# Kernel optimization log

Measured on AMD Instinct MI355X. Metric: run time of the kernel, lower is better.

Reference implementation:

```python
import jax, jax.numpy as jnp
import numpy as np

B, T, F = 256, 784, 1
H, D, C = 256, 1024, 10  # cell_size, dense_size, num_classes


def setup_inputs() -> dict:
    key = jax.random.key(0)
    ks = jax.random.split(key, 5)
    s = 0.05
    return {
        "X": jax.random.normal(ks[0], (B, T, F), jnp.float32),
        "W_lstm": jax.random.normal(ks[1], (F + H, 4 * H), jnp.float32) * s,
        "b_lstm": jnp.zeros((4 * H,), jnp.float32),
        "W_dense": jax.random.normal(ks[2], (H, D), jnp.float32) * s,
        "b_dense": jnp.zeros((D,), jnp.float32),
        "W_pred": jax.random.normal(ks[3], (D, C), jnp.float32) * s,
        "b_pred": jnp.zeros((C,), jnp.float32),
        "seq_length": T,
    }


def reference(X, W_lstm, b_lstm, W_dense, b_dense, W_pred, b_pred, seq_length):
    # TF LSTMCell: kernel [F+H, 4H], gate order (i, j, f, o), forget_bias=1.0
    b, t, f = X.shape
    h4 = W_lstm.shape[1]
    h = h4 // 4
    Wx, Wh = W_lstm[:f], W_lstm[f:]
    # Precompute input projections for all timesteps: [T, B, 4H]
    xproj = jnp.einsum('tbf,fg->tbg', jnp.transpose(X, (1, 0, 2)), Wx) + b_lstm

    def step(carry, xp):
        c, hst = carry
        gates = xp + hst @ Wh  # [B, 4H]
        i, j, fg, o = jnp.split(gates, 4, axis=-1)
        new_c = jax.nn.sigmoid(fg + 1.0) * c + jax.nn.sigmoid(i) * jnp.tanh(j)
        new_h = jax.nn.sigmoid(o) * jnp.tanh(new_c)
        return (new_c, new_h), None

    init = (jnp.zeros((b, h), X.dtype), jnp.zeros((b, h), X.dtype))
    (_, h_last), _ = jax.lax.scan(step, init, xproj)

    # Dropout in inference mode = identity
    dense = jax.nn.relu(h_last @ W_dense + b_dense)
    logits = dense @ W_pred + b_pred
    return logits
```

## Files before the change

kernel.cpp:

```cpp
#include <hip/hip_runtime.h>
#include <stdint.h>

#define TSEQ  784
#define BATCH 256
#define HID   256
#define DNS   1024
#define NCLS  10
#define NGRP  16
#define NSLC  8

typedef __attribute__((ext_vector_type(8))) short bf16x8_t;
typedef __attribute__((ext_vector_type(4))) float f32x4_t;

__device__ __forceinline__ float sigmoidf_(float x) { return 1.0f / (1.0f + __expf(-x)); }
__device__ __forceinline__ float tanhf_(float x) {
    float ax = fabsf(x);
    float e  = __expf(2.0f * ax);
    float r  = 1.0f - 2.0f / (e + 1.0f);
    return copysignf(r, x);
}
__device__ __forceinline__ uint32_t bf16rne(float f) {
    uint32_t u = __float_as_uint(f);
    return (u + 0x7FFFu + ((u >> 16) & 1u)) >> 16;
}
__device__ __forceinline__ float bf16tof(uint32_t h) { return __uint_as_float(h << 16); }

__global__ __launch_bounds__(256, 1)
void lstm_mfma(const float* __restrict__ X,
               const float* __restrict__ W_lstm,
               const float* __restrict__ b_lstm,
               uint32_t* __restrict__ hx,
               uint32_t* __restrict__ tags)
{
    __shared__ uint32_t WtU[32768];
    __shared__ uint32_t hA[4096];
    __shared__ float    gateL[4 * 32 * 17];

    const int tid  = threadIdx.x;
    const int lane = tid & 63;
    const int wid  = tid >> 6;
    const int cidx = lane & 15;
    const int kh   = lane >> 4;

    const int bid = blockIdx.x;
    const int s   = bid >> 4;
    const int g   = bid & 15;

    for (int idx = tid; idx < 8 * 16 * 128; idx += 256) {
        const int n  = idx >> 11;
        const int c  = (idx >> 7) & 15;
        const int dw = idx & 127;
        const int k0 = dw * 2;
        const int col = (n >> 1) * 256 + s * 32 + (n & 1) * 16 + c;
        const float w0 = W_lstm[(1 + k0) * 1024 + col];
        const float w1 = W_lstm[(2 + k0) * 1024 + col];
        const uint32_t h0 = bf16rne(w0), h1 = bf16rne(w1);
        const uint32_t l0 = bf16rne(w0 - bf16tof(h0));
        const uint32_t l1 = bf16rne(w1 - bf16tof(h1));
        const int kc = dw >> 2, rem = dw & 3;
        const int dwp = ((kc ^ (c & 7)) << 2) | rem;
        const int o = (n * 16 + c) * 128 + dwp;
        WtU[o]         = h0 | (h1 << 16);
        WtU[16384 + o] = l0 | (l1 << 16);
    }

    const int er = tid >> 4;
    const int eu = tid & 15;
    float wx0[4], wx1[4], bb0[4], bb1[4];
    #pragma unroll
    for (int q = 0; q < 4; ++q) {
        const int c0 = q * 256 + s * 32 + eu;
        wx0[q] = W_lstm[c0];      wx1[q] = W_lstm[c0 + 16];
        bb0[q] = b_lstm[c0];      bb1[q] = b_lstm[c0 + 16];
    }
    const float* xrow = X + (g * 16 + er) * TSEQ;
    float cc0 = 0.0f, cc1 = 0.0f;

    const int key = (cidx + (cidx >> 2)) & 3;
    const int kq  = (kh ^ key) << 2;

    __syncthreads();

    for (int t = 0; t < TSEQ; ++t) {
        if (t > 0 && wid == 0) {
            const uint32_t tt = (uint32_t)t;
            int guard = 1 << 22;
            bool ok;
            do {
                uint32_t v = __hip_atomic_load(&tags[g * 8 + (lane & 7)],
                                               __ATOMIC_RELAXED, __HIP_MEMORY_SCOPE_AGENT);
                ok = __all(v >= tt);
            } while (!ok && --guard);
        }
        __syncthreads();

        {
            const int bufr = t & 1;
            const unsigned long long* src =
                (const unsigned long long*)hx + (size_t)(bufr * NGRP + g) * 2048;
            unsigned long long v[8];
            #pragma unroll
            for (int j = 0; j < 8; ++j) {
                v[j] = __hip_atomic_load(&src[j * 256 + tid],
                                         __ATOMIC_RELAXED, __HIP_MEMORY_SCOPE_AGENT);
            }
            #pragma unroll
            for (int j = 0; j < 8; ++j) {
                const int m   = j * 256 + tid;
                const int kt  = m >> 8;
                const int lvl = (m >> 7) & 1;
                const int ci  = (m & 127) >> 3;
                const int ko  = (m & 7) * 2;
                const int khj = ko >> 2, dp = ko & 3;
                const int kyj = (ci + (ci >> 2)) & 3;
                const int dst = kt * 512 + lvl * 256 + ci * 16 + ((khj ^ kyj) << 2) + dp;
                *(unsigned long long*)&hA[dst] = v[j];
            }
        }
        __syncthreads();

        f32x4_t acc0 = {0.f, 0.f, 0.f, 0.f}, acc1 = acc0;
        #pragma unroll
        for (int kt = 0; kt < 8; ++kt) {
            bf16x8_t av_h = *reinterpret_cast<const bf16x8_t*>(&hA[kt * 512 + cidx * 16 + kq]);
            bf16x8_t av_l = *reinterpret_cast<const bf16x8_t*>(&hA[kt * 512 + 256 + cidx * 16 + kq]);
            const int kc = kt * 4 + kh;
            const int ob0 = ((wid * 2) * 16 + cidx) * 128 + ((kc ^ (cidx & 7)) << 2);
            const int ob1 = ((wid * 2 + 1) * 16 + cidx) * 128 + ((kc ^ (cidx & 7)) << 2);
            bf16x8_t bh0 = *reinterpret_cast<const bf16x8_t*>(&WtU[ob0]);
            bf16x8_t bl0 = *reinterpret_cast<const bf16x8_t*>(&WtU[16384 + ob0]);
            bf16x8_t bh1 = *reinterpret_cast<const bf16x8_t*>(&WtU[ob1]);
            bf16x8_t bl1 = *reinterpret_cast<const bf16x8_t*>(&WtU[16384 + ob1]);
            acc0 = __builtin_amdgcn_mfma_f32_16x16x32_bf16(av_h, bh0, acc0, 0, 0, 0);
            acc0 = __builtin_amdgcn_mfma_f32_16x16x32_bf16(av_h, bl0, acc0, 0, 0, 0);
            acc0 = __builtin_amdgcn_mfma_f32_16x16x32_bf16(av_l, bh0, acc0, 0, 0, 0);
            acc1 = __builtin_amdgcn_mfma_f32_16x16x32_bf16(av_h, bh1, acc1, 0, 0, 0);
            acc1 = __builtin_amdgcn_mfma_f32_16x16x32_bf16(av_h, bl1, acc1, 0, 0, 0);
            acc1 = __builtin_amdgcn_mfma_f32_16x16x32_bf16(av_l, bh1, acc1, 0, 0, 0);
        }

        #pragma unroll
        for (int reg = 0; reg < 4; ++reg) {
            gateL[(wid * 32 + cidx) * 17      + kh * 4 + reg] = acc0[reg];
            gateL[(wid * 32 + 16 + cidx) * 17 + kh * 4 + reg] = acc1[reg];
        }
        __syncthreads();

        const float xv = xrow[t];
        float g0[4], g1[4];
        #pragma unroll
        for (int q = 0; q < 4; ++q) {
            g0[q] = gateL[(q * 32 + eu) * 17 + er]      + xv * wx0[q] + bb0[q];
            g1[q] = gateL[(q * 32 + 16 + eu) * 17 + er] + xv * wx1[q] + bb1[q];
        }
        cc0 = fmaf(sigmoidf_(g0[2] + 1.0f), cc0, sigmoidf_(g0[0]) * tanhf_(g0[1]));
        const float h0 = sigmoidf_(g0[3]) * tanhf_(cc0);
        cc1 = fmaf(sigmoidf_(g1[2] + 1.0f), cc1, sigmoidf_(g1[0]) * tanhf_(g1[1]));
        const float h1 = sigmoidf_(g1[3]) * tanhf_(cc1);

        const float h0n = __shfl_xor(h0, 1, 64);
        const float h1n = __shfl_xor(h1, 1, 64);
        if ((eu & 1) == 0) {
            const int bufw  = (t + 1) & 1;
            const int basew = ((bufw * NGRP + g) * NSLC + s) * 512 + er * 16;
            const uint32_t hi0 = bf16rne(h0),  hi0n = bf16rne(h0n);
            const uint32_t hi1 = bf16rne(h1),  hi1n = bf16rne(h1n);
            const uint32_t lo0  = bf16rne(h0  - bf16tof(hi0));
            const uint32_t lo0n = bf16rne(h0n - bf16tof(hi0n));
            const uint32_t lo1  = bf16rne(h1  - bf16tof(hi1));
            const uint32_t lo1n = bf16rne(h1n - bf16tof(hi1n));
            const int D0 = eu >> 1, D1 = 8 + (eu >> 1);
            __hip_atomic_store(&hx[basew + D0], hi0 | (hi0n << 16),
                               __ATOMIC_RELAXED, __HIP_MEMORY_SCOPE_AGENT);
            __hip_atomic_store(&hx[basew + D1], hi1 | (hi1n << 16),
                               __ATOMIC_RELAXED, __HIP_MEMORY_SCOPE_AGENT);
            __hip_atomic_store(&hx[basew + 256 + D0], lo0 | (lo0n << 16),
                               __ATOMIC_RELAXED, __HIP_MEMORY_SCOPE_AGENT);
            __hip_atomic_store(&hx[basew + 256 + D1], lo1 | (lo1n << 16),
                               __ATOMIC_RELAXED, __HIP_MEMORY_SCOPE_AGENT);
        }
        __syncthreads();
        if (tid == 0) {
            __hip_atomic_store(&tags[g * 8 + s], (uint32_t)(t + 1),
                               __ATOMIC_RELAXED, __HIP_MEMORY_SCOPE_AGENT);
        }
    }
}

__global__ __launch_bounds__(256, 1)
void head_kernel(const uint32_t* __restrict__ hx,
                 const float* __restrict__ W_dense,
                 const float* __restrict__ b_dense,
                 const float* __restrict__ W_pred,
                 const float* __restrict__ b_pred,
                 float* __restrict__ out) {
    __shared__ float hs[HID];
    __shared__ float ds[DNS];
    __shared__ float red[4];

    const int b = blockIdx.x;
    const int g = b >> 4, er = b & 15;
    const int tid = threadIdx.x;

    {
        const int s  = tid >> 5;
        const int uu = tid & 31;
        const int base = (g * NSLC + s) * 512 + er * 16;
        const uint32_t dh = __hip_atomic_load(&hx[base + (uu >> 1)],
                                              __ATOMIC_RELAXED, __HIP_MEMORY_SCOPE_AGENT);
        const uint32_t dl = __hip_atomic_load(&hx[base + 256 + (uu >> 1)],
                                              __ATOMIC_RELAXED, __HIP_MEMORY_SCOPE_AGENT);
        const int sh = (uu & 1) * 16;
        hs[tid] = bf16tof((dh >> sh) & 0xFFFFu) + bf16tof((dl >> sh) & 0xFFFFu);
    }
    __syncthreads();

    for (int d = tid; d < DNS; d += 256) {
        float acc = b_dense[d];
        for (int k = 0; k < HID; k += 4) {
            float4 h4 = *reinterpret_cast<const float4*>(&hs[k]);
            acc = fmaf(h4.x, W_dense[(k + 0) * DNS + d], acc);
            acc = fmaf(h4.y, W_dense[(k + 1) * DNS + d], acc);
            acc = fmaf(h4.z, W_dense[(k + 2) * DNS + d], acc);
            acc = fmaf(h4.w, W_dense[(k + 3) * DNS + d], acc);
        }
        ds[d] = fmaxf(acc, 0.0f);
    }
    __syncthreads();

    const int wid = tid >> 6, lane = tid & 63;
    for (int c = 0; c < NCLS; ++c) {
        float p = 0.0f;
        for (int k = tid; k < DNS; k += 256) {
            p = fmaf(ds[k], W_pred[k * NCLS + c], p);
        }
        #pragma unroll
        for (int off = 32; off > 0; off >>= 1) {
            p += __shfl_down(p, off, 64);
        }
        if (lane == 0) red[wid] = p;
        __syncthreads();
        if (tid == 0) {
            out[b * NCLS + c] = red[0] + red[1] + red[2] + red[3] + b_pred[c];
        }
        __syncthreads();
    }
}

extern "C" void kernel_launch(void* const* d_in, const int* in_sizes, int n_in,
                              void* d_out, int out_size, void* d_ws, size_t ws_size,
                              hipStream_t stream) {
    const float* X       = (const float*)d_in[0];
    const float* W_lstm  = (const float*)d_in[1];
    const float* b_lstm  = (const float*)d_in[2];
    const float* W_dense = (const float*)d_in[3];
    const float* b_dense = (const float*)d_in[4];
    const float* W_pred  = (const float*)d_in[5];
    const float* b_pred  = (const float*)d_in[6];
    float* out = (float*)d_out;

    uint32_t* hx   = (uint32_t*)d_ws;
    uint32_t* tags = hx + 131072;

    hipMemsetAsync(hx, 0, NGRP * NSLC * 512 * sizeof(uint32_t), stream);
    hipMemsetAsync(tags, 0, NGRP * NSLC * sizeof(uint32_t), stream);

    lstm_mfma<<<NGRP * NSLC, 256, 0, stream>>>(X, W_lstm, b_lstm, hx, tags);
    head_kernel<<<BATCH, 256, 0, stream>>>(hx, W_dense, b_dense, W_pred, b_pred, out);
}
```

Baseline: 2.225 ms.

## Process two batch groups per block and load h operands directly from global

Halves the grid from 128 to 64 blocks, with each block handling two batch groups (A and B) over the same weight slice. Each weight fragment read from LDS now feeds twice the MFMA work, and each step waits on one tag poll. The recurrent h operand is now loaded straight from global into MFMA registers, removing the LDS staging pass and one barrier per step. The cost is more serial work per block on the critical recurrence path, fewer CUs in use, and higher register pressure.

New measurement: 4.983 ms. +124.0%, slower.

```diff
diff --git a/kernel.cpp b/kernel.cpp
--- a/kernel.cpp
+++ b/kernel.cpp
@@ -25,16 +25,21 @@
 }
 __device__ __forceinline__ float bf16tof(uint32_t h) { return __uint_as_float(h << 16); }
 
+union AF { uint32_t u[4]; unsigned long long q[2]; bf16x8_t v; };
+
+#define ALOAD(dst, ptr) \
+    dst = __hip_atomic_load((ptr), __ATOMIC_RELAXED, __HIP_MEMORY_SCOPE_AGENT)
+
 __global__ __launch_bounds__(256, 1)
-void lstm_mfma(const float* __restrict__ X,
-               const float* __restrict__ W_lstm,
-               const float* __restrict__ b_lstm,
-               uint32_t* __restrict__ hx,
-               uint32_t* __restrict__ tags)
+void lstm_mfma2(const float* __restrict__ X,
+                const float* __restrict__ W_lstm,
+                const float* __restrict__ b_lstm,
+                uint32_t* __restrict__ hx,
+                uint32_t* __restrict__ tags)
 {
     __shared__ uint32_t WtU[32768];
-    __shared__ uint32_t hA[4096];
-    __shared__ float    gateL[4 * 32 * 17];
+    __shared__ float    gateA[4 * 32 * 17];
+    __shared__ float    gateB[4 * 32 * 17];
 
     const int tid  = threadIdx.x;
     const int lane = tid & 63;
@@ -43,8 +48,9 @@
     const int kh   = lane >> 4;
 
     const int bid = blockIdx.x;
-    const int s   = bid >> 4;
-    const int g   = bid & 15;
+    const int s   = bid >> 3;
+    const int p   = bid & 7;
+    const int gA  = 2 * p, gB = 2 * p + 1;
 
     for (int idx = tid; idx < 8 * 16 * 128; idx += 256) {
         const int n  = idx >> 11;
@@ -73,11 +79,9 @@
         wx0[q] = W_lstm[c0];      wx1[q] = W_lstm[c0 + 16];
         bb0[q] = b_lstm[c0];      bb1[q] = b_lstm[c0 + 16];
     }
-    const float* xrow = X + (g * 16 + er) * TSEQ;
-    float cc0 = 0.0f, cc1 = 0.0f;
-
-    const int key = (cidx + (cidx >> 2)) & 3;
-    const int kq  = (kh ^ key) << 2;
+    const float* xrowA = X + (gA * 16 + er) * TSEQ;
+    const float* xrowB = X + (gB * 16 + er) * TSEQ;
+    float ccA0 = 0.f, ccA1 = 0.f, ccB0 = 0.f, ccB1 = 0.f;
 
     __syncthreads();
 
@@ -87,101 +91,133 @@
             int guard = 1 << 22;
             bool ok;
             do {
-                uint32_t v = __hip_atomic_load(&tags[g * 8 + (lane & 7)],
+                uint32_t v = __hip_atomic_load(&tags[p * 16 + (lane & 15)],
                                                __ATOMIC_RELAXED, __HIP_MEMORY_SCOPE_AGENT);
                 ok = __all(v >= tt);
             } while (!ok && --guard);
         }
         __syncthreads();
 
-        {
-            const int bufr = t & 1;
-            const unsigned long long* src =
-                (const unsigned long long*)hx + (size_t)(bufr * NGRP + g) * 2048;
-            unsigned long long v[8];
-            #pragma unroll
-            for (int j = 0; j < 8; ++j) {
-                v[j] = __hip_atomic_load(&src[j * 256 + tid],
-                                         __ATOMIC_RELAXED, __HIP_MEMORY_SCOPE_AGENT);
-            }
-            #pragma unroll
-            for (int j = 0; j < 8; ++j) {
-                const int m   = j * 256 + tid;
-                const int kt  = m >> 8;
-                const int lvl = (m >> 7) & 1;
-                const int ci  = (m & 127) >> 3;
-                const int ko  = (m & 7) * 2;
-                const int khj = ko >> 2, dp = ko & 3;
-                const int kyj = (ci + (ci >> 2)) & 3;
-                const int dst = kt * 512 + lvl * 256 + ci * 16 + ((khj ^ kyj) << 2) + dp;
-                *(unsigned long long*)&hA[dst] = v[j];
-            }
-        }
-        __syncthreads();
-
-        f32x4_t acc0 = {0.f, 0.f, 0.f, 0.f}, acc1 = acc0;
+        const int bufr = t & 1;
+        AF ahA[8], alA[8], ahB[8], alB[8];
         #pragma unroll
         for (int kt = 0; kt < 8; ++kt) {
-            bf16x8_t av_h = *reinterpret_cast<const bf16x8_t*>(&hA[kt * 512 + cidx * 16 + kq]);
-            bf16x8_t av_l = *reinterpret_cast<const bf16x8_t*>(&hA[kt * 512 + 256 + cidx * 16 + kq]);
-            const int kc = kt * 4 + kh;
+            const int baseA = ((bufr * NGRP + gA) * NSLC + kt) * 512 + cidx * 16 + kh * 4;
+            const int baseB = ((bufr * NGRP + gB) * NSLC + kt) * 512 + cidx * 16 + kh * 4;
+            const unsigned long long* pa = (const unsigned long long*)&hx[baseA];
+            const unsigned long long* pb = (const unsigned long long*)&hx[baseB];
+            ALOAD(ahA[kt].q[0], pa);       ALOAD(ahA[kt].q[1], pa + 1);
+            ALOAD(alA[kt].q[0], pa + 128); ALOAD(alA[kt].q[1], pa + 129);
+            ALOAD(ahB[kt].q[0], pb);       ALOAD(ahB[kt].q[1], pb + 1);
+            ALOAD(alB[kt].q[0], pb + 128); ALOAD(alB[kt].q[1], pb + 129);
+        }
+
+        f32x4_t aA0 = {0.f, 0.f, 0.f, 0.f}, aA1 = aA0, aB0 = aA0, aB1 = aA0;
+        #pragma unroll
+        for (int kt = 0; kt < 8; ++kt) {
+            const int kc  = kt * 4 + kh;
             const int ob0 = ((wid * 2) * 16 + cidx) * 128 + ((kc ^ (cidx & 7)) << 2);
             const int ob1 = ((wid * 2 + 1) * 16 + cidx) * 128 + ((kc ^ (cidx & 7)) << 2);
             bf16x8_t bh0 = *reinterpret_cast<const bf16x8_t*>(&WtU[ob0]);
             bf16x8_t bl0 = *reinterpret_cast<const bf16x8_t*>(&WtU[16384 + ob0]);
             bf16x8_t bh1 = *reinterpret_cast<const bf16x8_t*>(&WtU[ob1]);
             bf16x8_t bl1 = *reinterpret_cast<const bf16x8_t*>(&WtU[16384 + ob1]);
-            acc0 = __builtin_amdgcn_mfma_f32_16x16x32_bf16(av_h, bh0, acc0, 0, 0, 0);
-            acc0 = __builtin_amdgcn_mfma_f32_16x16x32_bf16(av_h, bl0, acc0, 0, 0, 0);
-            acc0 = __builtin_amdgcn_mfma_f32_16x16x32_bf16(av_l, bh0, acc0, 0, 0, 0);
-            acc1 = __builtin_amdgcn_mfma_f32_16x16x32_bf16(av_h, bh1, acc1, 0, 0, 0);
-            acc1 = __builtin_amdgcn_mfma_f32_16x16x32_bf16(av_h, bl1, acc1, 0, 0, 0);
-            acc1 = __builtin_amdgcn_mfma_f32_16x16x32_bf16(av_l, bh1, acc1, 0, 0, 0);
+            aA0 = __builtin_amdgcn_mfma_f32_16x16x32_bf16(ahA[kt].v, bh0, aA0, 0, 0, 0);
+            aA0 = __builtin_amdgcn_mfma_f32_16x16x32_bf16(ahA[kt].v, bl0, aA0, 0, 0, 0);
+            aA0 = __builtin_amdgcn_mfma_f32_16x16x32_bf16(alA[kt].v, bh0, aA0, 0, 0, 0);
+            aA1 = __builtin_amdgcn_mfma_f32_16x16x32_bf16(ahA[kt].v, bh1, aA1, 0, 0, 0);
+            aA1 = __builtin_amdgcn_mfma_f32_16x16x32_bf16(ahA[kt].v, bl1, aA1, 0, 0, 0);
+            aA1 = __builtin_amdgcn_mfma_f32_16x16x32_bf16(alA[kt].v, bh1, aA1, 0, 0, 0);
+            aB0 = __builtin_amdgcn_mfma_f32_16x16x32_bf16(ahB[kt].v, bh0, aB0, 0, 0, 0);
+            aB0 = __builtin_amdgcn_mfma_f32_16x16x32_bf16(ahB[kt].v, bl0, aB0, 0, 0, 0);
+            aB0 = __builtin_amdgcn_mfma_f32_16x16x32_bf16(alB[kt].v, bh0, aB0, 0, 0, 0);
+            aB1 = __builtin_amdgcn_mfma_f32_16x16x32_bf16(ahB[kt].v, bh1, aB1, 0, 0, 0);
+            aB1 = __builtin_amdgcn_mfma_f32_16x16x32_bf16(ahB[kt].v, bl1, aB1, 0, 0, 0);
+            aB1 = __builtin_amdgcn_mfma_f32_16x16x32_bf16(alB[kt].v, bh1, aB1, 0, 0, 0);
         }
 
         #pragma unroll
         for (int reg = 0; reg < 4; ++reg) {
-            gateL[(wid * 32 + cidx) * 17      + kh * 4 + reg] = acc0[reg];
-            gateL[(wid * 32 + 16 + cidx) * 17 + kh * 4 + reg] = acc1[reg];
-        }
-        __syncthreads();
-
-        const float xv = xrow[t];
-        float g0[4], g1[4];
-        #pragma unroll
-        for (int q = 0; q < 4; ++q) {
-            g0[q] = gateL[(q * 32 + eu) * 17 + er]      + xv * wx0[q] + bb0[q];
-            g1[q] = gateL[(q * 32 + 16 + eu) * 17 + er] + xv * wx1[q] + bb1[q];
-        }
-        cc0 = fmaf(sigmoidf_(g0[2] + 1.0f), cc0, sigmoidf_(g0[0]) * tanhf_(g0[1]));
-        const float h0 = sigmoidf_(g0[3]) * tanhf_(cc0);
-        cc1 = fmaf(sigmoidf_(g1[2] + 1.0f), cc1, sigmoidf_(g1[0]) * tanhf_(g1[1]));
-        const float h1 = sigmoidf_(g1[3]) * tanhf_(cc1);
-
-        const float h0n = __shfl_xor(h0, 1, 64);
-        const float h1n = __shfl_xor(h1, 1, 64);
-        if ((eu & 1) == 0) {
-            const int bufw  = (t + 1) & 1;
-            const int basew = ((bufw * NGRP + g) * NSLC + s) * 512 + er * 16;
-            const uint32_t hi0 = bf16rne(h0),  hi0n = bf16rne(h0n);
-            const uint32_t hi1 = bf16rne(h1),  hi1n = bf16rne(h1n);
-            const uint32_t lo0  = bf16rne(h0  - bf16tof(hi0));
-            const uint32_t lo0n = bf16rne(h0n - bf16tof(hi0n));
-            const uint32_t lo1  = bf16rne(h1  - bf16tof(hi1));
-            const uint32_t lo1n = bf16rne(h1n - bf16tof(hi1n));
-            const int D0 = eu >> 1, D1 = 8 + (eu >> 1);
-            __hip_atomic_store(&hx[basew + D0], hi0 | (hi0n << 16),
+            gateA[(wid * 32 + cidx) * 17      + kh * 4 + reg] = aA0[reg];
+            gateA[(wid * 32 + 16 + cidx) * 17 + kh * 4 + reg] = aA1[reg];
+            gateB[(wid * 32 + cidx) * 17      + kh * 4 + reg] = aB0[reg];
+            gateB[(wid * 32 + 16 + cidx) * 17 + kh * 4 + reg] = aB1[reg];
+        }
+        __syncthreads();
+
+        const int bufw = (t + 1) & 1;
+
+        {
+            const float xv = xrowA[t];
+            float g0[4], g1[4];
+            #pragma unroll
+            for (int q = 0; q < 4; ++q) {
+                g0[q] = gateA[(q * 32 + eu) * 17 + er]      + xv * wx0[q] + bb0[q];
+                g1[q] = gateA[(q * 32 + 16 + eu) * 17 + er] + xv * wx1[q] + bb1[q];
+            }
+            ccA0 = fmaf(sigmoidf_(g0[2] + 1.0f), ccA0, sigmoidf_(g0[0]) * tanhf_(g0[1]));
+            const float h0 = sigmoidf_(g0[3]) * tanhf_(ccA0);
+            ccA1 = fmaf(sigmoidf_(g1[2] + 1.0f), ccA1, sigmoidf_(g1[0]) * tanhf_(g1[1]));
+            const float h1 = sigmoidf_(g1[3]) * tanhf_(ccA1);
+            const float h0n = __shfl_xor(h0, 1, 64);
+            const float h1n = __shfl_xor(h1, 1, 64);
+            if ((eu & 1) == 0) {
+                const int basew = ((bufw * NGRP + gA) * NSLC + s) * 512 + er * 16;
+                const uint32_t hi0 = bf16rne(h0),  hi0n = bf16rne(h0n);
+                const uint32_t hi1 = bf16rne(h1),  hi1n = bf16rne(h1n);
+                const uint32_t lo0  = bf16rne(h0  - bf16tof(hi0));
+                const uint32_t lo0n = bf16rne(h0n - bf16tof(hi0n));
+                const uint32_t lo1  = bf16rne(h1  - bf16tof(hi1));
+                const uint32_t lo1n = bf16rne(h1n - bf16tof(hi1n));
+                const int D0 = eu >> 1, D1 = 8 + (eu >> 1);
+                __hip_atomic_store(&hx[basew + D0], hi0 | (hi0n << 16),
+                                   __ATOMIC_RELAXED, __HIP_MEMORY_SCOPE_AGENT);
+                __hip_atomic_store(&hx[basew + D1], hi1 | (hi1n << 16),
+                                   __ATOMIC_RELAXED, __HIP_MEMORY_SCOPE_AGENT);
+                __hip_atomic_store(&hx[basew + 256 + D0], lo0 | (lo0n << 16),
+                                   __ATOMIC_RELAXED, __HIP_MEMORY_SCOPE_AGENT);
+                __hip_atomic_store(&hx[basew + 256 + D1], lo1 | (lo1n << 16),
+                                   __ATOMIC_RELAXED, __HIP_MEMORY_SCOPE_AGENT);
+            }
+        }
+        {
+            const float xv = xrowB[t];
+            float g0[4], g1[4];
+            #pragma unroll
+            for (int q = 0; q < 4; ++q) {
+                g0[q] = gateB[(q * 32 + eu) * 17 + er]      + xv * wx0[q] + bb0[q];
+                g1[q] = gateB[(q * 32 + 16 + eu) * 17 + er] + xv * wx1[q] + bb1[q];
+            }
+            ccB0 = fmaf(sigmoidf_(g0[2] + 1.0f), ccB0, sigmoidf_(g0[0]) * tanhf_(g0[1]));
+            const float h0 = sigmoidf_(g0[3]) * tanhf_(ccB0);
+            ccB1 = fmaf(sigmoidf_(g1[2] + 1.0f), ccB1, sigmoidf_(g1[0]) * tanhf_(g1[1]));
+            const float h1 = sigmoidf_(g1[3]) * tanhf_(ccB1);
+            const float h0n = __shfl_xor(h0, 1, 64);
+            const float h1n = __shfl_xor(h1, 1, 64);
+            if ((eu & 1) == 0) {
+                const int basew = ((bufw * NGRP + gB) * NSLC + s) * 512 + er * 16;
+                const uint32_t hi0 = bf16rne(h0),  hi0n = bf16rne(h0n);
+                const uint32_t hi1 = bf16rne(h1),  hi1n = bf16rne(h1n);
+                const uint32_t lo0  = bf16rne(h0  - bf16tof(hi0));
+                const uint32_t lo0n = bf16rne(h0n - bf16tof(hi0n));
+                const uint32_t lo1  = bf16rne(h1  - bf16tof(hi1));
+                const uint32_t lo1n = bf16rne(h1n - bf16tof(hi1n));
+                const int D0 = eu >> 1, D1 = 8 + (eu >> 1);
+                __hip_atomic_store(&hx[basew + D0], hi0 | (hi0n << 16),
+                                   __ATOMIC_RELAXED, __HIP_MEMORY_SCOPE_AGENT);
+                __hip_atomic_store(&hx[basew + D1], hi1 | (hi1n << 16),
+                                   __ATOMIC_RELAXED, __HIP_MEMORY_SCOPE_AGENT);
+                __hip_atomic_store(&hx[basew + 256 + D0], lo0 | (lo0n << 16),
+                                   __ATOMIC_RELAXED, __HIP_MEMORY_SCOPE_AGENT);
+                __hip_atomic_store(&hx[basew + 256 + D1], lo1 | (lo1n << 16),
+                                   __ATOMIC_RELAXED, __HIP_MEMORY_SCOPE_AGENT);
+            }
+        }
+        __syncthreads();
+        if (tid == 0) {
+            __hip_atomic_store(&tags[gA * 8 + s], (uint32_t)(t + 1),
                                __ATOMIC_RELAXED, __HIP_MEMORY_SCOPE_AGENT);
-            __hip_atomic_store(&hx[basew + D1], hi1 | (hi1n << 16),
-                               __ATOMIC_RELAXED, __HIP_MEMORY_SCOPE_AGENT);
-            __hip_atomic_store(&hx[basew + 256 + D0], lo0 | (lo0n << 16),
-                               __ATOMIC_RELAXED, __HIP_MEMORY_SCOPE_AGENT);
-            __hip_atomic_store(&hx[basew + 256 + D1], lo1 | (lo1n << 16),
-                               __ATOMIC_RELAXED, __HIP_MEMORY_SCOPE_AGENT);
-        }
-        __syncthreads();
-        if (tid == 0) {
-            __hip_atomic_store(&tags[g * 8 + s], (uint32_t)(t + 1),
+            __hip_atomic_store(&tags[gB * 8 + s], (uint32_t)(t + 1),
                                __ATOMIC_RELAXED, __HIP_MEMORY_SCOPE_AGENT);
         }
     }
@@ -265,6 +301,6 @@
     hipMemsetAsync(hx, 0, NGRP * NSLC * 512 * sizeof(uint32_t), stream);
     hipMemsetAsync(tags, 0, NGRP * NSLC * sizeof(uint32_t), stream);
 
-    lstm_mfma<<<NGRP * NSLC, 256, 0, stream>>>(X, W_lstm, b_lstm, hx, tags);
+    lstm_mfma2<<<NSLC * 8, 256, 0, stream>>>(X, W_lstm, b_lstm, hx, tags);
     head_kernel<<<BATCH, 256, 0, stream>>>(hx, W_dense, b_dense, W_pred, b_pred, out);
 }
```

## Interleave two batch groups per block to overlap recurrent sync latency

Applied to the files above, without the earlier changes.

The LSTM kernel now launches 64 blocks instead of 128, and each block runs two independent batch groups (g and g+8) in alternation for every timestep. The weight slice in LDS is shared by both groups. The aim is that while one group waits on its peers' hidden-state tags, the other group's work is already progressing, hiding cross-block sync latency. The swizzle on the hA LDS staging was also removed, which may bring back bank conflicts, and each block now does twice the serial work per step.

Measured after the change: 3.759 ms. +69.0%, slower.

```diff
diff --git a/kernel.cpp b/kernel.cpp
--- a/kernel.cpp
+++ b/kernel.cpp
@@ -25,12 +25,119 @@
 }
 __device__ __forceinline__ float bf16tof(uint32_t h) { return __uint_as_float(h << 16); }
 
+#define ALOAD(dst, ptr) \
+    dst = __hip_atomic_load((ptr), __ATOMIC_RELAXED, __HIP_MEMORY_SCOPE_AGENT)
+
+__device__ __forceinline__ void lstm_phase(
+    int t, int g, int s, int tid, int lane, int wid, int cidx, int kh,
+    const uint32_t* WtU, uint32_t* hA, float* gateL,
+    const float* xrow, float& cc0, float& cc1,
+    const float* wx0, const float* wx1, const float* bb0, const float* bb1,
+    uint32_t* hx, uint32_t* tags)
+{
+    if (t > 0 && wid == 0) {
+        const uint32_t tt = (uint32_t)t;
+        int guard = 1 << 22;
+        bool ok;
+        do {
+            uint32_t v = __hip_atomic_load(&tags[g * 8 + (lane & 7)],
+                                           __ATOMIC_RELAXED, __HIP_MEMORY_SCOPE_AGENT);
+            ok = __all(v >= tt);
+        } while (!ok && --guard);
+    }
+    __syncthreads();
+
+    {
+        const int bufr = t & 1;
+        const unsigned long long* src =
+            (const unsigned long long*)hx + (size_t)(bufr * NGRP + g) * 2048;
+        unsigned long long v[8];
+        #pragma unroll
+        for (int j = 0; j < 8; ++j) {
+            ALOAD(v[j], &src[j * 256 + tid]);
+        }
+        #pragma unroll
+        for (int j = 0; j < 8; ++j) {
+            *(unsigned long long*)&hA[(j * 256 + tid) * 2] = v[j];
+        }
+    }
+    __syncthreads();
+
+    f32x4_t acc0 = {0.f, 0.f, 0.f, 0.f}, acc1 = acc0;
+    #pragma unroll
+    for (int kt = 0; kt < 8; ++kt) {
+        bf16x8_t av_h = *reinterpret_cast<const bf16x8_t*>(&hA[kt * 512 + cidx * 16 + kh * 4]);
+        bf16x8_t av_l = *reinterpret_cast<const bf16x8_t*>(&hA[kt * 512 + 256 + cidx * 16 + kh * 4]);
+        const int kc  = kt * 4 + kh;
+        const int ob0 = ((wid * 2) * 16 + cidx) * 128 + ((kc ^ (cidx & 7)) << 2);
+        const int ob1 = ((wid * 2 + 1) * 16 + cidx) * 128 + ((kc ^ (cidx & 7)) << 2);
+        bf16x8_t bh0 = *reinterpret_cast<const bf16x8_t*>(&WtU[ob0]);
+        bf16x8_t bl0 = *reinterpret_cast<const bf16x8_t*>(&WtU[16384 + ob0]);
+        bf16x8_t bh1 = *reinterpret_cast<const bf16x8_t*>(&WtU[ob1]);
+        bf16x8_t bl1 = *reinterpret_cast<const bf16x8_t*>(&WtU[16384 + ob1]);
+        acc0 = __builtin_amdgcn_mfma_f32_16x16x32_bf16(av_h, bh0, acc0, 0, 0, 0);
+        acc0 = __builtin_amdgcn_mfma_f32_16x16x32_bf16(av_h, bl0, acc0, 0, 0, 0);
+        acc0 = __builtin_amdgcn_mfma_f32_16x16x32_bf16(av_l, bh0, acc0, 0, 0, 0);
+        acc1 = __builtin_amdgcn_mfma_f32_16x16x32_bf16(av_h, bh1, acc1, 0, 0, 0);
+        acc1 = __builtin_amdgcn_mfma_f32_16x16x32_bf16(av_h, bl1, acc1, 0, 0, 0);
+        acc1 = __builtin_amdgcn_mfma_f32_16x16x32_bf16(av_l, bh1, acc1, 0, 0, 0);
+    }
+
+    #pragma unroll
+    for (int reg = 0; reg < 4; ++reg) {
+        gateL[(wid * 32 + cidx) * 17      + kh * 4 + reg] = acc0[reg];
+        gateL[(wid * 32 + 16 + cidx) * 17 + kh * 4 + reg] = acc1[reg];
+    }
+    __syncthreads();
+
+    const int er = tid >> 4;
+    const int eu = tid & 15;
+    const float xv = xrow[t];
+    float g0[4], g1[4];
+    #pragma unroll
+    for (int q = 0; q < 4; ++q) {
+        g0[q] = gateL[(q * 32 + eu) * 17 + er]      + xv * wx0[q] + bb0[q];
+        g1[q] = gateL[(q * 32 + 16 + eu) * 17 + er] + xv * wx1[q] + bb1[q];
+    }
+    cc0 = fmaf(sigmoidf_(g0[2] + 1.0f), cc0, sigmoidf_(g0[0]) * tanhf_(g0[1]));
+    const float h0 = sigmoidf_(g0[3]) * tanhf_(cc0);
+    cc1 = fmaf(sigmoidf_(g1[2] + 1.0f), cc1, sigmoidf_(g1[0]) * tanhf_(g1[1]));
+    const float h1 = sigmoidf_(g1[3]) * tanhf_(cc1);
+
+    const float h0n = __shfl_xor(h0, 1, 64);
+    const float h1n = __shfl_xor(h1, 1, 64);
+    if ((eu & 1) == 0) {
+        const int bufw  = (t + 1) & 1;
+        const int basew = ((bufw * NGRP + g) * NSLC + s) * 512 + er * 16;
+        const uint32_t hi0 = bf16rne(h0),  hi0n = bf16rne(h0n);
+        const uint32_t hi1 = bf16rne(h1),  hi1n = bf16rne(h1n);
+        const uint32_t lo0  = bf16rne(h0  - bf16tof(hi0));
+        const uint32_t lo0n = bf16rne(h0n - bf16tof(hi0n));
+        const uint32_t lo1  = bf16rne(h1  - bf16tof(hi1));
+        const uint32_t lo1n = bf16rne(h1n - bf16tof(hi1n));
+        const int D0 = eu >> 1, D1 = 8 + (eu >> 1);
+        __hip_atomic_store(&hx[basew + D0], hi0 | (hi0n << 16),
+                           __ATOMIC_RELAXED, __HIP_MEMORY_SCOPE_AGENT);
+        __hip_atomic_store(&hx[basew + D1], hi1 | (hi1n << 16),
+                           __ATOMIC_RELAXED, __HIP_MEMORY_SCOPE_AGENT);
+        __hip_atomic_store(&hx[basew + 256 + D0], lo0 | (lo0n << 16),
+                           __ATOMIC_RELAXED, __HIP_MEMORY_SCOPE_AGENT);
+        __hip_atomic_store(&hx[basew + 256 + D1], lo1 | (lo1n << 16),
+                           __ATOMIC_RELAXED, __HIP_MEMORY_SCOPE_AGENT);
+    }
+    __syncthreads();
+    if (tid == 0) {
+        __hip_atomic_store(&tags[g * 8 + s], (uint32_t)(t + 1),
+                           __ATOMIC_RELAXED, __HIP_MEMORY_SCOPE_AGENT);
+    }
+}
+
 __global__ __launch_bounds__(256, 1)
-void lstm_mfma(const float* __restrict__ X,
-               const float* __restrict__ W_lstm,
-               const float* __restrict__ b_lstm,
-               uint32_t* __restrict__ hx,
-               uint32_t* __restrict__ tags)
+void lstm_mfma5(const float* __restrict__ X,
+                const float* __restrict__ W_lstm,
+                const float* __restrict__ b_lstm,
+                uint32_t* __restrict__ hx,
+                uint32_t* __restrict__ tags)
 {
     __shared__ uint32_t WtU[32768];
     __shared__ uint32_t hA[4096];
@@ -43,8 +150,9 @@
     const int kh   = lane >> 4;
 
     const int bid = blockIdx.x;
-    const int s   = bid >> 4;
-    const int g   = bid & 15;
+    const int p   = bid & 7;
+    const int s   = bid >> 3;
+    const int gA  = p, gB = p + 8;
 
     for (int idx = tid; idx < 8 * 16 * 128; idx += 256) {
         const int n  = idx >> 11;
@@ -73,117 +181,17 @@
         wx0[q] = W_lstm[c0];      wx1[q] = W_lstm[c0 + 16];
         bb0[q] = b_lstm[c0];      bb1[q] = b_lstm[c0 + 16];
     }
-    const float* xrow = X + (g * 16 + er) * TSEQ;
-    float cc0 = 0.0f, cc1 = 0.0f;
-
-    const int key = (cidx + (cidx >> 2)) & 3;
-    const int kq  = (kh ^ key) << 2;
+    const float* xrowA = X + (gA * 16 + er) * TSEQ;
+    const float* xrowB = X + (gB * 16 + er) * TSEQ;
+    float ccA0 = 0.f, ccA1 = 0.f, ccB0 = 0.f, ccB1 = 0.f;
 
     __syncthreads();
 
     for (int t = 0; t < TSEQ; ++t) {
-        if (t > 0 && wid == 0) {
-            const uint32_t tt = (uint32_t)t;
-            int guard = 1 << 22;
-            bool ok;
-            do {
-                uint32_t v = __hip_atomic_load(&tags[g * 8 + (lane & 7)],
-                                               __ATOMIC_RELAXED, __HIP_MEMORY_SCOPE_AGENT);
-                ok = __all(v >= tt);
-            } while (!ok && --guard);
-        }
-        __syncthreads();
-
-        {
-            const int bufr = t & 1;
-            const unsigned long long* src =
-                (const unsigned long long*)hx + (size_t)(bufr * NGRP + g) * 2048;
-            unsigned long long v[8];
-            #pragma unroll
-            for (int j = 0; j < 8; ++j) {
-                v[j] = __hip_atomic_load(&src[j * 256 + tid],
-                                         __ATOMIC_RELAXED, __HIP_MEMORY_SCOPE_AGENT);
-            }
-            #pragma unroll
-            for (int j = 0; j < 8; ++j) {
-                const int m   = j * 256 + tid;
-                const int kt  = m >> 8;
-                const int lvl = (m >> 7) & 1;
-                const int ci  = (m & 127) >> 3;
-                const int ko  = (m & 7) * 2;
-                const int khj = ko >> 2, dp = ko & 3;
-                const int kyj = (ci + (ci >> 2)) & 3;
-                const int dst = kt * 512 + lvl * 256 + ci * 16 + ((khj ^ kyj) << 2) + dp;
-                *(unsigned long long*)&hA[dst] = v[j];
-            }
-        }
-        __syncthreads();
-
-        f32x4_t acc0 = {0.f, 0.f, 0.f, 0.f}, acc1 = acc0;
-        #pragma unroll
-        for (int kt = 0; kt < 8; ++kt) {
-            bf16x8_t av_h = *reinterpret_cast<const bf16x8_t*>(&hA[kt * 512 + cidx * 16 + kq]);
-            bf16x8_t av_l = *reinterpret_cast<const bf16x8_t*>(&hA[kt * 512 + 256 + cidx * 16 + kq]);
-            const int kc = kt * 4 + kh;
-            const int ob0 = ((wid * 2) * 16 + cidx) * 128 + ((kc ^ (cidx & 7)) << 2);
-            const int ob1 = ((wid * 2 + 1) * 16 + cidx) * 128 + ((kc ^ (cidx & 7)) << 2);
-            bf16x8_t bh0 = *reinterpret_cast<const bf16x8_t*>(&WtU[ob0]);
-            bf16x8_t bl0 = *reinterpret_cast<const bf16x8_t*>(&WtU[16384 + ob0]);
-            bf16x8_t bh1 = *reinterpret_cast<const bf16x8_t*>(&WtU[ob1]);
-            bf16x8_t bl1 = *reinterpret_cast<const bf16x8_t*>(&WtU[16384 + ob1]);
-            acc0 = __builtin_amdgcn_mfma_f32_16x16x32_bf16(av_h, bh0, acc0, 0, 0, 0);
-            acc0 = __builtin_amdgcn_mfma_f32_16x16x32_bf16(av_h, bl0, acc0, 0, 0, 0);
-            acc0 = __builtin_amdgcn_mfma_f32_16x16x32_bf16(av_l, bh0, acc0, 0, 0, 0);
-            acc1 = __builtin_amdgcn_mfma_f32_16x16x32_bf16(av_h, bh1, acc1, 0, 0, 0);
-            acc1 = __builtin_amdgcn_mfma_f32_16x16x32_bf16(av_h, bl1, acc1, 0, 0, 0);
-            acc1 = __builtin_amdgcn_mfma_f32_16x16x32_bf16(av_l, bh1, acc1, 0, 0, 0);
-        }
-
-        #pragma unroll
-        for (int reg = 0; reg < 4; ++reg) {
-            gateL[(wid * 32 + cidx) * 17      + kh * 4 + reg] = acc0[reg];
-            gateL[(wid * 32 + 16 + cidx) * 17 + kh * 4 + reg] = acc1[reg];
-        }
-        __syncthreads();
-
-        const float xv = xrow[t];
-        float g0[4], g1[4];
-        #pragma unroll
-        for (int q = 0; q < 4; ++q) {
-            g0[q] = gateL[(q * 32 + eu) * 17 + er]      + xv * wx0[q] + bb0[q];
-            g1[q] = gateL[(q * 32 + 16 + eu) * 17 + er] + xv * wx1[q] + bb1[q];
-        }
-        cc0 = fmaf(sigmoidf_(g0[2] + 1.0f), cc0, sigmoidf_(g0[0]) * tanhf_(g0[1]));
-        const float h0 = sigmoidf_(g0[3]) * tanhf_(cc0);
-        cc1 = fmaf(sigmoidf_(g1[2] + 1.0f), cc1, sigmoidf_(g1[0]) * tanhf_(g1[1]));
-        const float h1 = sigmoidf_(g1[3]) * tanhf_(cc1);
-
-        const float h0n = __shfl_xor(h0, 1, 64);
-        const float h1n = __shfl_xor(h1, 1, 64);
-        if ((eu & 1) == 0) {
-            const int bufw  = (t + 1) & 1;
-            const int basew = ((bufw * NGRP + g) * NSLC + s) * 512 + er * 16;
-            const uint32_t hi0 = bf16rne(h0),  hi0n = bf16rne(h0n);
-            const uint32_t hi1 = bf16rne(h1),  hi1n = bf16rne(h1n);
-            const uint32_t lo0  = bf16rne(h0  - bf16tof(hi0));
-            const uint32_t lo0n = bf16rne(h0n - bf16tof(hi0n));
-            const uint32_t lo1  = bf16rne(h1  - bf16tof(hi1));
-            const uint32_t lo1n = bf16rne(h1n - bf16tof(hi1n));
-            const int D0 = eu >> 1, D1 = 8 + (eu >> 1);
-            __hip_atomic_store(&hx[basew + D0], hi0 | (hi0n << 16),
-                               __ATOMIC_RELAXED, __HIP_MEMORY_SCOPE_AGENT);
-            __hip_atomic_store(&hx[basew + D1], hi1 | (hi1n << 16),
-                               __ATOMIC_RELAXED, __HIP_MEMORY_SCOPE_AGENT);
-            __hip_atomic_store(&hx[basew + 256 + D0], lo0 | (lo0n << 16),
-                               __ATOMIC_RELAXED, __HIP_MEMORY_SCOPE_AGENT);
-            __hip_atomic_store(&hx[basew + 256 + D1], lo1 | (lo1n << 16),
-                               __ATOMIC_RELAXED, __HIP_MEMORY_SCOPE_AGENT);
-        }
-        __syncthreads();
-        if (tid == 0) {
-            __hip_atomic_store(&tags[g * 8 + s], (uint32_t)(t + 1),
-                               __ATOMIC_RELAXED, __HIP_MEMORY_SCOPE_AGENT);
-        }
+        lstm_phase(t, gA, s, tid, lane, wid, cidx, kh, WtU, hA, gateL,
+                   xrowA, ccA0, ccA1, wx0, wx1, bb0, bb1, hx, tags);
+        lstm_phase(t, gB, s, tid, lane, wid, cidx, kh, WtU, hA, gateL,
+                   xrowB, ccB0, ccB1, wx0, wx1, bb0, bb1, hx, tags);
     }
 }
 
@@ -206,10 +214,9 @@
         const int s  = tid >> 5;
         const int uu = tid & 31;
         const int base = (g * NSLC + s) * 512 + er * 16;
-        const uint32_t dh = __hip_atomic_load(&hx[base + (uu >> 1)],
-                                              __ATOMIC_RELAXED, __HIP_MEMORY_SCOPE_AGENT);
-        const uint32_t dl = __hip_atomic_load(&hx[base + 256 + (uu >> 1)],
-                                              __ATOMIC_RELAXED, __HIP_MEMORY_SCOPE_AGENT);
+        uint32_t dh, dl;
+        ALOAD(dh, &hx[base + (uu >> 1)]);
+        ALOAD(dl, &hx[base + 256 + (uu >> 1)]);
         const int sh = (uu & 1) * 16;
         hs[tid] = bf16tof((dh >> sh) & 0xFFFFu) + bf16tof((dl >> sh) & 0xFFFFu);
     }
@@ -265,6 +272,6 @@
     hipMemsetAsync(hx, 0, NGRP * NSLC * 512 * sizeof(uint32_t), stream);
     hipMemsetAsync(tags, 0, NGRP * NSLC * sizeof(uint32_t), stream);
 
-    lstm_mfma<<<NGRP * NSLC, 256, 0, stream>>>(X, W_lstm, b_lstm, hx, tags);
+    lstm_mfma5<<<64, 256, 0, stream>>>(X, W_lstm, b_lstm, hx, tags);
     head_kernel<<<BATCH, 256, 0, stream>>>(hx, W_dense, b_dense, W_pred, b_pred, out);
 }
```

## Replace per-block tag barrier with per-wave atomic counter synchronization

Applied to the files above, without the earlier changes.

Each timestep previously had one wave poll eight per-slice tags and then hit a block-wide barrier, plus a second barrier before thread 0 published its tag. Now each wave waits on a single per-group counter that must reach 32 increments per step, and after its stores drain each wave adds its own increment, removing both __syncthreads calls from the step. This lets waves proceed independently and cuts intra-block barrier latency on the serial recurrence. In exchange, all waves spin on global memory and the counter takes more atomic traffic. Without the block barrier, ordering of the shared-memory hA writes and reads across waves now relies on the code between them.

After: 2.522 ms. 1.13x slower.

```diff
diff --git a/kernel.cpp b/kernel.cpp
--- a/kernel.cpp
+++ b/kernel.cpp
@@ -30,7 +30,7 @@
                const float* __restrict__ W_lstm,
                const float* __restrict__ b_lstm,
                uint32_t* __restrict__ hx,
-               uint32_t* __restrict__ tags)
+               uint32_t* __restrict__ cnt)
 {
     __shared__ uint32_t WtU[32768];
     __shared__ uint32_t hA[4096];
@@ -78,21 +78,20 @@
 
     const int key = (cidx + (cidx >> 2)) & 3;
     const int kq  = (kh ^ key) << 2;
+    uint32_t* const cptr = &cnt[g * 32];
 
     __syncthreads();
 
     for (int t = 0; t < TSEQ; ++t) {
-        if (t > 0 && wid == 0) {
-            const uint32_t tt = (uint32_t)t;
+        if (t > 0) {
+            const uint32_t tgt = 32u * (uint32_t)t;
             int guard = 1 << 22;
-            bool ok;
-            do {
-                uint32_t v = __hip_atomic_load(&tags[g * 8 + (lane & 7)],
-                                               __ATOMIC_RELAXED, __HIP_MEMORY_SCOPE_AGENT);
-                ok = __all(v >= tt);
-            } while (!ok && --guard);
-        }
-        __syncthreads();
+            while (__hip_atomic_load(cptr, __ATOMIC_RELAXED,
+                                     __HIP_MEMORY_SCOPE_AGENT) < tgt) {
+                if (--guard == 0) break;
+            }
+        }
+        asm volatile("" ::: "memory");
 
         {
             const int bufr = t & 1;
@@ -179,10 +178,9 @@
             __hip_atomic_store(&hx[basew + 256 + D1], lo1 | (lo1n << 16),
                                __ATOMIC_RELAXED, __HIP_MEMORY_SCOPE_AGENT);
         }
-        __syncthreads();
-        if (tid == 0) {
-            __hip_atomic_store(&tags[g * 8 + s], (uint32_t)(t + 1),
-                               __ATOMIC_RELAXED, __HIP_MEMORY_SCOPE_AGENT);
+        asm volatile("s_waitcnt vmcnt(0)" ::: "memory");
+        if (lane == 0) {
+            __hip_atomic_fetch_add(cptr, 1u, __ATOMIC_RELAXED, __HIP_MEMORY_SCOPE_AGENT);
         }
     }
 }
@@ -259,12 +257,12 @@
     const float* b_pred  = (const float*)d_in[6];
     float* out = (float*)d_out;
 
-    uint32_t* hx   = (uint32_t*)d_ws;
-    uint32_t* tags = hx + 131072;
+    uint32_t* hx  = (uint32_t*)d_ws;
+    uint32_t* cnt = hx + 131072;
 
     hipMemsetAsync(hx, 0, NGRP * NSLC * 512 * sizeof(uint32_t), stream);
-    hipMemsetAsync(tags, 0, NGRP * NSLC * sizeof(uint32_t), stream);
-
-    lstm_mfma<<<NGRP * NSLC, 256, 0, stream>>>(X, W_lstm, b_lstm, hx, tags);
+    hipMemsetAsync(cnt, 0, NGRP * 32 * sizeof(uint32_t), stream);
+
+    lstm_mfma<<<NGRP * NSLC, 256, 0, stream>>>(X, W_lstm, b_lstm, hx, cnt);
     head_kernel<<<BATCH, 256, 0, stream>>>(hx, W_dense, b_dense, W_pred, b_pred, out);
 }
```
